# Optimization experiments

Measured on AMD Instinct MI355X. Metric: run time of the kernel, lower is better.

## Reference

```python
import jax, jax.numpy as jnp
import numpy as np

H, E, DFF = 1024, 8, 4096


def setup_inputs() -> dict:
    key = jax.random.key(0)
    ks = jax.random.split(key, 7)
    s = lambda *shape: 1.0 / np.sqrt(shape[-2] if len(shape) > 1 else shape[-1])
    x = jax.random.normal(ks[0], (2, 2048, H), dtype=jnp.float32)
    Wr = jax.random.normal(ks[1], (H, E), dtype=jnp.float32) * (1.0 / np.sqrt(H))
    br = jnp.zeros((E,), dtype=jnp.float32)
    W1 = jax.random.normal(ks[2], (E, H, DFF), dtype=jnp.float32) * (1.0 / np.sqrt(H))
    b1 = jnp.zeros((E, DFF), dtype=jnp.float32)
    W2 = jax.random.normal(ks[3], (E, DFF, H), dtype=jnp.float32) * (1.0 / np.sqrt(DFF))
    b2 = jnp.zeros((E, H), dtype=jnp.float32)
    return {"x": x, "Wr": Wr, "br": br, "W1": W1, "b1": b1, "W2": W2, "b2": b2}


def reference(x, Wr, br, W1, b1, W2, b2):
    B, S, Hd = x.shape
    n_exp = W1.shape[0]
    xt = x.reshape(-1, Hd)                      # (T, H)
    logits = xt @ Wr + br                       # (T, E)
    probs = jax.nn.softmax(logits, axis=-1)
    gate = jnp.max(probs, axis=-1)              # (T,) top-1 gate value
    idx = jnp.argmax(probs, axis=-1)            # (T,) chosen expert
    # dense all-expert FFN, then one-hot combine (vectorized equivalent of per-token loop)
    h1 = jnp.maximum(jnp.einsum('th,ehf->etf', xt, W1) + b1[:, None, :], 0.0)  # (E,T,DFF)
    ye = jnp.einsum('etf,efh->eth', h1, W2) + b2[:, None, :]                   # (E,T,H)
    onehot = jax.nn.one_hot(idx, n_exp, dtype=xt.dtype)                        # (T,E)
    y = jnp.einsum('te,eth->th', onehot, ye) * gate[:, None]                   # (T,H)
    return y.reshape(B, S, Hd)
```

## Files before the change

kernel.cpp:

```cpp
#include <hip/hip_runtime.h>
#include <stdint.h>

typedef unsigned short u16;
typedef __attribute__((ext_vector_type(8))) short s16x8;
typedef __attribute__((ext_vector_type(4))) float f32x4;
typedef __attribute__((ext_vector_type(4))) unsigned uint4v;

#define NEXP 8
#define HD 1024
#define DFF 4096
#define BM 128
#define BN 128
#define BK 64

#define TILE_U16 (BM * BK)

__device__ __forceinline__ u16 f2bf(float f) {
  union { float f; unsigned u; } c; c.f = f;
  unsigned r = c.u + 0x7fffu + ((c.u >> 16) & 1u);
  return (u16)(r >> 16);
}

__device__ __forceinline__ unsigned cvtpk(float a, float b) {
  unsigned r;
  asm("v_cvt_pk_bf16_f32 %0, %1, %2" : "=v"(r) : "v"(a), "v"(b));
  return r;
}

__device__ __forceinline__ void gload_lds16(const void* g, const void* l) {
  __builtin_amdgcn_global_load_lds(
      (const __attribute__((address_space(1))) unsigned int*)(uintptr_t)g,
      (__attribute__((address_space(3))) unsigned int*)(unsigned)(uintptr_t)l,
      16, 0, 0);
}

template <int K, int N>
__device__ __forceinline__ void convt_gl(const float* __restrict__ W,
    u16* __restrict__ Wp, int idx, float* __restrict__ Tf) {
  const int e = idx >> 9;
  const int ti = idx & 511;
  const int k0 = (ti % (K / 128)) * 128;
  const int n0 = (ti / (K / 128)) * 64;
  const int t = threadIdx.x;
  const float* src = W + (size_t)e * K * N + (size_t)k0 * N + n0;
#pragma unroll
  for (int c = 0; c < 8; ++c) {
    int slot = c * 256 + t;
    gload_lds16(src + (size_t)(slot >> 4) * N + (slot & 15) * 4, Tf + slot * 4);
  }
  __syncthreads();
  const int p = t >> 7, nl = (t & 127) >> 1, kh = t & 1;
  float v[32];
#pragma unroll
  for (int j = 0; j < 32; ++j)
    v[j] = Tf[(p * 64 + kh * 32 + j) * 64 + nl];
  uint4v q0, q1, q2, q3;
#pragma unroll
  for (int a = 0; a < 4; ++a) {
    q0[a] = cvtpk(v[2 * a], v[2 * a + 1]);
    q1[a] = cvtpk(v[8 + 2 * a], v[9 + 2 * a]);
    q2[a] = cvtpk(v[16 + 2 * a], v[17 + 2 * a]);
    q3[a] = cvtpk(v[24 + 2 * a], v[25 + 2 * a]);
  }
  u16* d = Wp + (size_t)e * K * N + ((size_t)(k0 / 64 + p)) * N * 64
         + (size_t)(n0 + nl) * 64 + kh * 32;
  *(uint4v*)d = q0;
  *(uint4v*)(d + 8) = q1;
  *(uint4v*)(d + 16) = q2;
  *(uint4v*)(d + 24) = q3;
}

__global__ __launch_bounds__(256) void prep1_k(
    const float* __restrict__ x, const float* __restrict__ Wr,
    const float* __restrict__ br,
    int* __restrict__ tok_exp, float* __restrict__ tok_gate,
    const float* __restrict__ W1, u16* __restrict__ W1t,
    u16* __restrict__ Xbf, int T) {
  __shared__ __align__(16) float Tf[128 * 64];
  const int bid = blockIdx.x;
  const int NBR = T / 4;
  if (bid >= NBR) {
    convt_gl<HD, DFF>(W1, W1t, bid - NBR, Tf);
    return;
  }
  const int w = threadIdx.x >> 6, l = threadIdx.x & 63;
  const int t = bid * 4 + w;
  const float4* xr = (const float4*)(x + (size_t)t * HD);
  float acc[NEXP];
#pragma unroll
  for (int j = 0; j < NEXP; ++j) acc[j] = 0.f;
#pragma unroll
  for (int i = 0; i < 4; ++i) {
    float4 v = xr[l + i * 64];
    unsigned pa = cvtpk(v.x, v.y), pb = cvtpk(v.z, v.w);
    *(uint2*)&Xbf[(size_t)t * HD + (l + i * 64) * 4] = make_uint2(pa, pb);
    const int h = (l + i * 64) * 4;
    const float* w0 = Wr + (size_t)h * NEXP;
#pragma unroll
    for (int c = 0; c < 4; ++c) {
      float xv = (c == 0) ? v.x : (c == 1) ? v.y : (c == 2) ? v.z : v.w;
      const float4* wr4 = (const float4*)(w0 + c * NEXP);
      float4 a = wr4[0], b = wr4[1];
      acc[0] += xv * a.x; acc[1] += xv * a.y; acc[2] += xv * a.z; acc[3] += xv * a.w;
      acc[4] += xv * b.x; acc[5] += xv * b.y; acc[6] += xv * b.z; acc[7] += xv * b.w;
    }
  }
#pragma unroll
  for (int j = 0; j < NEXP; ++j)
#pragma unroll
    for (int off = 32; off > 0; off >>= 1) acc[j] += __shfl_xor(acc[j], off);
  if (l == 0) {
    float lg[NEXP];
    float best = acc[0] + br[0]; int bi = 0;
    lg[0] = best;
#pragma unroll
    for (int j = 1; j < NEXP; ++j) {
      lg[j] = acc[j] + br[j];
      if (lg[j] > best) { best = lg[j]; bi = j; }
    }
    float s = 0.f;
#pragma unroll
    for (int j = 0; j < NEXP; ++j) s += expf(lg[j] - best);
    tok_exp[t] = bi;
    tok_gate[t] = 1.0f / s;
  }
}

__global__ __launch_bounds__(64) void scan_k(const int* __restrict__ tok_exp, int T,
    int* __restrict__ seg, int* __restrict__ cursor,
    int* __restrict__ ntile, int* __restrict__ tile_e, int* __restrict__ tile_m) {
  const int l = threadIdx.x;
  int cnt[NEXP];
#pragma unroll
  for (int j = 0; j < NEXP; ++j) cnt[j] = 0;
  for (int i = l; i < T; i += 64) {
    int e = tok_exp[i];
#pragma unroll
    for (int j = 0; j < NEXP; ++j) cnt[j] += (e == j) ? 1 : 0;
  }
#pragma unroll
  for (int j = 0; j < NEXP; ++j)
#pragma unroll
    for (int off = 32; off > 0; off >>= 1) cnt[j] += __shfl_xor(cnt[j], off);
  if (l == 0) {
    int s = 0, nt = 0;
#pragma unroll
    for (int e = 0; e < NEXP; ++e) {
      seg[e] = s; cursor[e] = s;
      int c = cnt[e];
      for (int m = 0; m < c; m += BM) { tile_e[nt] = e; tile_m[nt] = m; ++nt; }
      s += c;
    }
    seg[NEXP] = s;
    ntile[0] = nt;
  }
}

__global__ __launch_bounds__(256) void gatherlite_k(const int* __restrict__ tok_exp,
    const float* __restrict__ tok_gate, int* __restrict__ cursor,
    int* __restrict__ perm, float* __restrict__ gatep) {
  const int t = blockIdx.x * 256 + threadIdx.x;
  int e = tok_exp[t];
  int pos = atomicAdd(&cursor[e], 1);
  perm[pos] = t;
  gatep[pos] = tok_gate[t];
}

template <int KD, int ND, int EPI, int KSPLIT, bool AIND>
__device__ __forceinline__ void gemm_body(
    u16* __restrict__ sh,
    const u16* __restrict__ A, const u16* __restrict__ Bp,
    const float* __restrict__ bias, const int* __restrict__ seg,
    const int* __restrict__ ntile, const int* __restrict__ tile_e,
    const int* __restrict__ tile_m, const int* __restrict__ perm,
    u16* __restrict__ H1out, float* __restrict__ Pt,
    int bx, int by, int ks) {
  if (by >= ntile[0]) return;
  const int e  = tile_e[by];
  const int m0 = tile_m[by];
  const int s0 = seg[e];
  const int cnt = seg[e + 1] - s0;
  const int n0 = bx * BN;
  constexpr int NT = (KD / KSPLIT) / BK;
  constexpr size_t BSTEP = (size_t)ND * 64;
  const int kbase = ks * (KD / KSPLIT);

  const int t = threadIdx.x;
  const int l = t & 63, w = t >> 6;
  const int wr = w >> 1, wc = w & 1;

  const f32x4 fzero = {0.f, 0.f, 0.f, 0.f};
  f32x4 acc[4][4];
#pragma unroll
  for (int i = 0; i < 4; ++i)
#pragma unroll
    for (int j = 0; j < 4; ++j) acc[i][j] = fzero;

  const int sub = t & 7, r8 = t >> 3;
  const int koff = (sub ^ (r8 & 7)) * 8;
  int aoff[4], boff[4];
  const u16* bte = Bp + (size_t)e * ND * KD;
#pragma unroll
  for (int c = 0; c < 4; ++c) {
    int row = c * 32 + r8;
    int rg = m0 + row; if (rg >= cnt) rg = cnt - 1;
    int arow;
    if constexpr (AIND) arow = perm[s0 + rg];
    else arow = s0 + rg;
    aoff[c] = arow * KD + kbase + koff;
    boff[c] = (kbase / 64) * (int)BSTEP + (n0 + row) * 64 + koff;
  }

  u16* Ac = sh;
  u16* Bc = sh + TILE_U16;
  u16* An = sh + 2 * TILE_U16;
  u16* Bn = sh + 3 * TILE_U16;

#define STAGE(pa, pb, tt) do { \
    _Pragma("unroll") for (int c_ = 0; c_ < 4; ++c_) \
      gload_lds16(A + (size_t)aoff[c_] + (size_t)(tt) * BK, (pa) + (c_ * 256 + t) * 8); \
    _Pragma("unroll") for (int c_ = 0; c_ < 4; ++c_) \
      gload_lds16(bte + (size_t)boff[c_] + (size_t)(tt) * BSTEP, (pb) + (c_ * 256 + t) * 8); \
  } while (0)

#define COMPUTE(pa, pb) do { \
    _Pragma("unroll") for (int s_ = 0; s_ < 2; ++s_) { \
      const int fo_ = ((s_ * 4 + (l >> 4)) ^ (l & 7)) * 8; \
      s16x8 af_[4], bf_[4]; \
      _Pragma("unroll") for (int mi_ = 0; mi_ < 4; ++mi_) \
        af_[mi_] = *(const s16x8*)&(pa)[(wr * 64 + mi_ * 16 + (l & 15)) * BK + fo_]; \
      _Pragma("unroll") for (int ni_ = 0; ni_ < 4; ++ni_) \
        bf_[ni_] = *(const s16x8*)&(pb)[(wc * 64 + ni_ * 16 + (l & 15)) * BK + fo_]; \
      _Pragma("unroll") for (int mi_ = 0; mi_ < 4; ++mi_) \
        _Pragma("unroll") for (int ni_ = 0; ni_ < 4; ++ni_) \
          acc[mi_][ni_] = __builtin_amdgcn_mfma_f32_16x16x32_bf16(af_[mi_], bf_[ni_], acc[mi_][ni_], 0, 0, 0); \
    } \
  } while (0)

  STAGE(Ac, Bc, 0);
  __syncthreads();
  for (int tt = 0; tt < NT; ++tt) {
    if (tt + 1 < NT) STAGE(An, Bn, tt + 1);
    COMPUTE(Ac, Bc);
    if (tt + 1 < NT) {
      __syncthreads();
      u16* xp;
      xp = Ac; Ac = An; An = xp;
      xp = Bc; Bc = Bn; Bn = xp;
    }
  }

#undef STAGE
#undef COMPUTE

  const int lr = (l >> 4) * 4;
  const int lc = l & 15;

  if constexpr (EPI == 0) {
    float bv2[4];
#pragma unroll
    for (int ni = 0; ni < 4; ++ni)
      bv2[ni] = bias[(size_t)e * ND + n0 + wc * 64 + ni * 16 + lc];
#pragma unroll
    for (int mi = 0; mi < 4; ++mi) {
#pragma unroll
      for (int r = 0; r < 4; ++r) {
        int row = m0 + wr * 64 + mi * 16 + lr + r;
        if (row < cnt) {
          u16* hrow = H1out + (size_t)(s0 + row) * ND + n0 + wc * 64;
#pragma unroll
          for (int ni = 0; ni < 4; ++ni) {
            float v = acc[mi][ni][r] + bv2[ni];
            v = v > 0.f ? v : 0.f;
            hrow[ni * 16 + lc] = f2bf(v);
          }
        }
      }
    }
  } else {
    const int totT = seg[NEXP];
#pragma unroll
    for (int mi = 0; mi < 4; ++mi) {
#pragma unroll
      for (int r = 0; r < 4; ++r) {
        int row = m0 + wr * 64 + mi * 16 + lr + r;
        if (row < cnt) {
          float* prow = Pt + ((size_t)ks * totT + s0 + row) * ND + n0 + wc * 64;
#pragma unroll
          for (int ni = 0; ni < 4; ++ni)
            prow[ni * 16 + lc] = acc[mi][ni][r];
        }
      }
    }
  }
}

__global__ __launch_bounds__(256, 2) void gemm1_fused_k(
    const u16* __restrict__ Xbf, const u16* __restrict__ W1t,
    const float* __restrict__ b1, const int* __restrict__ seg,
    const int* __restrict__ ntile, const int* __restrict__ tile_e,
    const int* __restrict__ tile_m, const int* __restrict__ perm,
    u16* __restrict__ H1,
    const float* __restrict__ W2, u16* __restrict__ W2t, int ng1) {
  __shared__ __align__(16) u16 sh[4 * TILE_U16];
  const int bid = blockIdx.x;
  if (bid < ng1) {
    gemm_body<HD, DFF, 0, 1, true>(sh, Xbf, W1t, b1, seg, ntile, tile_e, tile_m,
                                   perm, H1, nullptr,
                                   bid % (DFF / BN), bid / (DFF / BN), 0);
  } else {
    convt_gl<DFF, HD>(W2, W2t, bid - ng1, (float*)sh);
  }
}

__global__ __launch_bounds__(256, 2) void gemm2_k(
    const u16* __restrict__ H1, const u16* __restrict__ W2t,
    const int* __restrict__ seg, const int* __restrict__ ntile,
    const int* __restrict__ tile_e, const int* __restrict__ tile_m,
    float* __restrict__ Pt) {
  __shared__ __align__(16) u16 sh[4 * TILE_U16];
  gemm_body<DFF, HD, 2, 2, false>(sh, H1, W2t, nullptr, seg, ntile, tile_e,
                                  tile_m, nullptr, nullptr, Pt,
                                  blockIdx.x, blockIdx.y, blockIdx.z);
}

__global__ __launch_bounds__(256) void reduce_k(const float* __restrict__ Pt,
    const float* __restrict__ b2, const int* __restrict__ perm,
    const float* __restrict__ gatep, const int* __restrict__ tok_exp,
    float* __restrict__ out) {
  const int pos = blockIdx.x;
  const int totT = gridDim.x;
  const int tok = perm[pos];
  const float g = gatep[pos];
  const int e = tok_exp[tok];
  const int h = threadIdx.x * 4;
  float4 s = *(const float4*)(Pt + ((size_t)0 * totT + pos) * HD + h);
  float4 p = *(const float4*)(Pt + ((size_t)1 * totT + pos) * HD + h);
  s.x += p.x; s.y += p.y; s.z += p.z; s.w += p.w;
  float4 b = *(const float4*)(b2 + (size_t)e * HD + h);
  float4 o;
  o.x = (s.x + b.x) * g; o.y = (s.y + b.y) * g;
  o.z = (s.z + b.z) * g; o.w = (s.w + b.w) * g;
  *(float4*)(out + (size_t)tok * HD + h) = o;
}

extern "C" void kernel_launch(void* const* d_in, const int* in_sizes, int n_in,
                              void* d_out, int out_size, void* d_ws, size_t ws_size,
                              hipStream_t stream) {
  const float* x  = (const float*)d_in[0];
  const float* Wr = (const float*)d_in[1];
  const float* br = (const float*)d_in[2];
  const float* W1 = (const float*)d_in[3];
  const float* b1 = (const float*)d_in[4];
  const float* W2 = (const float*)d_in[5];
  const float* b2 = (const float*)d_in[6];
  float* out = (float*)d_out;

  const int T = in_sizes[0] / HD;
  char* ws = (char*)d_ws;
  int*   cursor   = (int*)(ws + 64);
  int*   seg      = (int*)(ws + 128);
  int*   ntile    = (int*)(ws + 192);
  int*   tile_e   = (int*)(ws + 256);
  int*   tile_m   = (int*)(ws + 512);
  int*   tok_exp  = (int*)(ws + 1024);
  float* tok_gate = (float*)(ws + 1024 + 4 * (size_t)T);
  int*   perm     = (int*)(ws + 1024 + 8 * (size_t)T);
  float* gatep    = (float*)(ws + 1024 + 12 * (size_t)T);
  u16*   Xbf      = (u16*)(ws + 1024 + 16 * (size_t)T);
  u16*   H1       = (u16*)(ws + 1024 + 16 * (size_t)T + 2 * (size_t)T * HD);
  size_t off2     = 1024 + 16 * (size_t)T + 2 * (size_t)T * HD + 2 * (size_t)T * DFF;
  u16*   W1t      = (u16*)(ws + off2);
  u16*   W2t      = (u16*)(ws + off2 + 2 * (size_t)NEXP * HD * DFF);
  float* Pt       = (float*)W1t;

  const int NBR = T / 4;
  const int NCT = 512 * NEXP;
  hipLaunchKernelGGL(prep1_k, dim3(NBR + NCT), dim3(256), 0, stream,
                     x, Wr, br, tok_exp, tok_gate, W1, W1t, Xbf, T);
  hipLaunchKernelGGL(scan_k, dim3(1), dim3(64), 0, stream,
                     tok_exp, T, seg, cursor, ntile, tile_e, tile_m);
  hipLaunchKernelGGL(gatherlite_k, dim3(T / 256), dim3(256), 0, stream,
                     tok_exp, tok_gate, cursor, perm, gatep);
  const int maxtile = (T + BM - 1) / BM + NEXP - 1;
  const int ng1 = (DFF / BN) * maxtile;
  hipLaunchKernelGGL(gemm1_fused_k, dim3(ng1 + NCT), dim3(256), 0, stream,
                     Xbf, W1t, b1, seg, ntile, tile_e, tile_m, perm, H1, W2, W2t, ng1);
  hipLaunchKernelGGL(gemm2_k, dim3(HD / BN, maxtile, 2), dim3(256), 0, stream,
                     H1, W2t, seg, ntile, tile_e, tile_m, Pt);
  hipLaunchKernelGGL(reduce_k, dim3(T), dim3(256), 0, stream, Pt, b2, perm, gatep, tok_exp, out);
}
```

Measured before the change: 251.7 us.

## Double-buffer weight transpose tiles, four tiles per block with overlapped loads

The fp32-to-bf16 weight transpose now processes four tiles per block instead of one. It ping-pongs two LDS buffers so the global-to-LDS load of the next tile overlaps the convert-and-store of the current one. This cuts block count and launch overhead and hides load latency. The cost is doubled LDS in prep1_k, which may reduce occupancy, and fewer blocks to spread across the GPU.

```diff
diff --git a/kernel.cpp b/kernel.cpp
--- a/kernel.cpp
+++ b/kernel.cpp
@@ -35,39 +35,62 @@
 }
 
 template <int K, int N>
-__device__ __forceinline__ void convt_gl(const float* __restrict__ W,
-    u16* __restrict__ Wp, int idx, float* __restrict__ Tf) {
-  const int e = idx >> 9;
-  const int ti = idx & 511;
-  const int k0 = (ti % (K / 128)) * 128;
-  const int n0 = (ti / (K / 128)) * 64;
+__device__ __forceinline__ void convt_quad_gl(const float* __restrict__ W,
+    u16* __restrict__ Wp, int b0, float* __restrict__ Tf0, float* __restrict__ Tf1) {
   const int t = threadIdx.x;
-  const float* src = W + (size_t)e * K * N + (size_t)k0 * N + n0;
-#pragma unroll
-  for (int c = 0; c < 8; ++c) {
-    int slot = c * 256 + t;
-    gload_lds16(src + (size_t)(slot >> 4) * N + (slot & 15) * 4, Tf + slot * 4);
-  }
+  constexpr int TPE = (K / 128) * (N / 64);
+  const float* sp[4];
+  u16* dp[4];
+#pragma unroll
+  for (int i = 0; i < 4; ++i) {
+    int idx = b0 + i;
+    int e = idx / TPE, ti = idx % TPE;
+    int k0 = (ti % (K / 128)) * 128, n0 = (ti / (K / 128)) * 64;
+    sp[i] = W + (size_t)e * K * N + (size_t)k0 * N + n0;
+    dp[i] = Wp + (size_t)e * K * N + (size_t)(k0 / 64) * N * 64 + (size_t)n0 * 64;
+  }
+  const int p = t >> 7, nl = (t & 127) >> 1, kh = t & 1;
+
+#define STAGE_T(Tf, i) do { \
+    _Pragma("unroll") for (int c_ = 0; c_ < 8; ++c_) { \
+      int slot_ = c_ * 256 + t; \
+      gload_lds16(sp[i] + (size_t)(slot_ >> 4) * N + (slot_ & 15) * 4, (Tf) + slot_ * 4); \
+    } \
+  } while (0)
+
+#define PHASE2_T(Tf, i) do { \
+    float v_[32]; \
+    _Pragma("unroll") for (int j_ = 0; j_ < 32; ++j_) \
+      v_[j_] = (Tf)[(p * 64 + kh * 32 + j_) * 64 + nl]; \
+    uint4v q0_, q1_, q2_, q3_; \
+    _Pragma("unroll") for (int a_ = 0; a_ < 4; ++a_) { \
+      q0_[a_] = cvtpk(v_[2 * a_], v_[2 * a_ + 1]); \
+      q1_[a_] = cvtpk(v_[8 + 2 * a_], v_[9 + 2 * a_]); \
+      q2_[a_] = cvtpk(v_[16 + 2 * a_], v_[17 + 2 * a_]); \
+      q3_[a_] = cvtpk(v_[24 + 2 * a_], v_[25 + 2 * a_]); \
+    } \
+    u16* d_ = dp[i] + (size_t)p * N * 64 + (size_t)nl * 64 + kh * 32; \
+    *(uint4v*)d_ = q0_; \
+    *(uint4v*)(d_ + 8) = q1_; \
+    *(uint4v*)(d_ + 16) = q2_; \
+    *(uint4v*)(d_ + 24) = q3_; \
+  } while (0)
+
+  STAGE_T(Tf0, 0);
   __syncthreads();
-  const int p = t >> 7, nl = (t & 127) >> 1, kh = t & 1;
-  float v[32];
-#pragma unroll
-  for (int j = 0; j < 32; ++j)
-    v[j] = Tf[(p * 64 + kh * 32 + j) * 64 + nl];
-  uint4v q0, q1, q2, q3;
-#pragma unroll
-  for (int a = 0; a < 4; ++a) {
-    q0[a] = cvtpk(v[2 * a], v[2 * a + 1]);
-    q1[a] = cvtpk(v[8 + 2 * a], v[9 + 2 * a]);
-    q2[a] = cvtpk(v[16 + 2 * a], v[17 + 2 * a]);
-    q3[a] = cvtpk(v[24 + 2 * a], v[25 + 2 * a]);
-  }
-  u16* d = Wp + (size_t)e * K * N + ((size_t)(k0 / 64 + p)) * N * 64
-         + (size_t)(n0 + nl) * 64 + kh * 32;
-  *(uint4v*)d = q0;
-  *(uint4v*)(d + 8) = q1;
-  *(uint4v*)(d + 16) = q2;
-  *(uint4v*)(d + 24) = q3;
+  STAGE_T(Tf1, 1);
+  PHASE2_T(Tf0, 0);
+  __syncthreads();
+  STAGE_T(Tf0, 2);
+  PHASE2_T(Tf1, 1);
+  __syncthreads();
+  STAGE_T(Tf1, 3);
+  PHASE2_T(Tf0, 2);
+  __syncthreads();
+  PHASE2_T(Tf1, 3);
+
+#undef STAGE_T
+#undef PHASE2_T
 }
 
 __global__ __launch_bounds__(256) void prep1_k(
@@ -76,11 +99,11 @@
     int* __restrict__ tok_exp, float* __restrict__ tok_gate,
     const float* __restrict__ W1, u16* __restrict__ W1t,
     u16* __restrict__ Xbf, int T) {
-  __shared__ __align__(16) float Tf[128 * 64];
+  __shared__ __align__(16) float Tf[2][128 * 64];
   const int bid = blockIdx.x;
   const int NBR = T / 4;
   if (bid >= NBR) {
-    convt_gl<HD, DFF>(W1, W1t, bid - NBR, Tf);
+    convt_quad_gl<HD, DFF>(W1, W1t, (bid - NBR) * 4, Tf[0], Tf[1]);
     return;
   }
   const int w = threadIdx.x >> 6, l = threadIdx.x & 63;
@@ -309,7 +332,8 @@
                                    perm, H1, nullptr,
                                    bid % (DFF / BN), bid / (DFF / BN), 0);
   } else {
-    convt_gl<DFF, HD>(W2, W2t, bid - ng1, (float*)sh);
+    convt_quad_gl<DFF, HD>(W2, W2t, (bid - ng1) * 4,
+                           (float*)sh, (float*)(sh + 2 * TILE_U16));
   }
 }
 
@@ -375,8 +399,8 @@
   float* Pt       = (float*)W1t;
 
   const int NBR = T / 4;
-  const int NCT = 512 * NEXP;
-  hipLaunchKernelGGL(prep1_k, dim3(NBR + NCT), dim3(256), 0, stream,
+  const int NCB = 512 * NEXP / 4;
+  hipLaunchKernelGGL(prep1_k, dim3(NBR + NCB), dim3(256), 0, stream,
                      x, Wr, br, tok_exp, tok_gate, W1, W1t, Xbf, T);
   hipLaunchKernelGGL(scan_k, dim3(1), dim3(64), 0, stream,
                      tok_exp, T, seg, cursor, ntile, tile_e, tile_m);
@@ -384,7 +408,7 @@
                      tok_exp, tok_gate, cursor, perm, gatep);
   const int maxtile = (T + BM - 1) / BM + NEXP - 1;
   const int ng1 = (DFF / BN) * maxtile;
-  hipLaunchKernelGGL(gemm1_fused_k, dim3(ng1 + NCT), dim3(256), 0, stream,
+  hipLaunchKernelGGL(gemm1_fused_k, dim3(ng1 + NCB), dim3(256), 0, stream,
                      Xbf, W1t, b1, seg, ntile, tile_e, tile_m, perm, H1, W2, W2t, ng1);
   hipLaunchKernelGGL(gemm2_k, dim3(HD / BN, maxtile, 2), dim3(256), 0, stream,
                      H1, W2t, seg, ntile, tile_e, tile_m, Pt);
```

After: 258.9 us. 1.03x slower.
